# Kernel optimization log

Measured on AMD Instinct MI355X. Metric: run time of the kernel, lower is better.

## Reference

```python
import jax, jax.numpy as jnp
import numpy as np

N, D, C = 16384, 2048, 2048


def setup_inputs() -> dict:
    key = jax.random.key(0)
    k1, k2, k3, k4 = jax.random.split(key, 4)
    inputs = jax.random.normal(k1, (N, D), dtype=jnp.float32)
    centers = jax.random.normal(k2, (C, D), dtype=jnp.float32)
    # fit() sets gamma = 1/(n_features * var); emulate a small positive scalar
    gamma = jax.random.uniform(k3, (1,), dtype=jnp.float32) / D
    normalization = jax.random.normal(k4, (C, C), dtype=jnp.float32) / jnp.sqrt(jnp.float32(C))
    return {"inputs": inputs, "centers": centers, "gamma": gamma, "normalization": normalization}


def reference(inputs, centers, gamma, normalization):
    x = inputs.reshape(inputs.shape[0], -1)
    x_sq = jnp.sum(x * x, axis=1, keepdims=True)          # [N, 1]
    c_sq = jnp.sum(centers * centers, axis=1)[None, :]    # [1, C]
    sq_dists = x_sq + c_sq - 2.0 * (x @ centers.T)        # [N, C]
    densities = jnp.exp(-gamma[0] * sq_dists)             # Gaussian kernel
    return densities @ normalization                      # [N, C]
```

## Files before the change

### kernel.cpp

```cpp
#include <hip/hip_runtime.h>
#include <hip/hip_bf16.h>


#define N_ROWS 16384
#define D_DIM  2048
#define C_DIM  2048

typedef __attribute__((ext_vector_type(4))) float f32x4;
typedef __attribute__((ext_vector_type(8))) _Float16 f16x8;

__device__ __forceinline__ void load_lds16(const void* g, void* l) {
  __builtin_amdgcn_global_load_lds(
      (const __attribute__((address_space(1))) unsigned int*)g,
      (__attribute__((address_space(3))) unsigned int*)l, 16, 0, 0);
}

__global__ void prep_rows(const float* __restrict__ src,
                          _Float16* __restrict__ dst,
                          float* __restrict__ sq) {
  const int row = blockIdx.x;
  const int t = threadIdx.x;
  const float* p = src + (size_t)row * D_DIM + t * 8;
  float4 v0 = ((const float4*)p)[0];
  float4 v1 = ((const float4*)p)[1];
  float vals[8] = {v0.x, v0.y, v0.z, v0.w, v1.x, v1.y, v1.z, v1.w};
  float ss = 0.f;
  f16x8 h;
#pragma unroll
  for (int j = 0; j < 8; ++j) {
    ss += vals[j] * vals[j];
    h[j] = (_Float16)vals[j];
  }
  *(f16x8*)(dst + (size_t)row * D_DIM + t * 8) = h;
  __shared__ float red[4];
  const int lane = t & 63, wave = t >> 6;
#pragma unroll
  for (int off = 32; off > 0; off >>= 1) ss += __shfl_down(ss, off);
  if (lane == 0) red[wave] = ss;
  __syncthreads();
  if (t == 0) sq[row] = red[0] + red[1] + red[2] + red[3];
}

__global__ void prep_wt(const float* __restrict__ W,
                        _Float16* __restrict__ WT) {
  __shared__ float tile[64][65];
  const int bc = blockIdx.x >> 5;
  const int bj = blockIdx.x & 31;
  const int t = threadIdx.x;
#pragma unroll
  for (int i = 0; i < 16; ++i) {
    int idx = i * 256 + t;
    int r = idx >> 6, c = idx & 63;
    tile[r][c] = W[(size_t)(bc * 64 + r) * C_DIM + bj * 64 + c];
  }
  __syncthreads();
#pragma unroll
  for (int i = 0; i < 16; ++i) {
    int idx = i * 256 + t;
    int r2 = idx >> 6, c2 = idx & 63;
    WT[(size_t)(bj * 64 + r2) * C_DIM + bc * 64 + c2] = (_Float16)tile[c2][r2];
  }
}

__global__ __launch_bounds__(256, 2) void gemm1(
    const _Float16* __restrict__ Xh, const _Float16* __restrict__ Ch,
    const float* __restrict__ x_sq, const float* __restrict__ c_sq,
    const float* __restrict__ gamma,
    _Float16* __restrict__ Ph) {
  constexpr int K = D_DIM;
  __shared__ _Float16 As[128 * 64];
  __shared__ _Float16 Bs[128 * 64];
  const int tid = threadIdx.x;
  const int lane = tid & 63, wave = tid >> 6;
  const int wr = wave >> 1, wc = wave & 1;
  const int nwg = gridDim.x;
  const int cpx = nwg >> 3;
  const int wgid = (blockIdx.x & 7) * cpx + (blockIdx.x >> 3);
  const int bcol = wgid & 15;
  const int brow = wgid >> 4;
  const int fr = lane & 15, fq = lane >> 4;
  f32x4 acc[4][4] = {};
  const float g = gamma[0];

  const char* Abase = (const char*)(Xh + (size_t)brow * 128 * K);
  const char* Bbase = (const char*)(Ch + (size_t)bcol * 128 * K);
  for (int kt = 0; kt < K; kt += 64) {
#pragma unroll
    for (int r = 0; r < 4; ++r) {
      int base = r * 4096 + wave * 1024;
      int bo = base + lane * 16;
      int row = bo >> 7;
      int inrow = (bo & 127) ^ ((row & 7) << 4);
      load_lds16(Abase + (size_t)row * K * 2 + kt * 2 + inrow, (char*)As + base);
      load_lds16(Bbase + (size_t)row * K * 2 + kt * 2 + inrow, (char*)Bs + base);
    }
    __syncthreads();
#pragma unroll
    for (int ks = 0; ks < 64; ks += 32) {
      f16x8 af[4], bfr[4];
#pragma unroll
      for (int m = 0; m < 4; ++m) {
        int row = wr * 64 + m * 16 + fr;
        int pb = row * 128 + (((ks + fq * 8) * 2) ^ ((row & 7) << 4));
        af[m] = *(const f16x8*)((const char*)As + pb);
      }
#pragma unroll
      for (int n = 0; n < 4; ++n) {
        int row = wc * 64 + n * 16 + fr;
        int pb = row * 128 + (((ks + fq * 8) * 2) ^ ((row & 7) << 4));
        bfr[n] = *(const f16x8*)((const char*)Bs + pb);
      }
#pragma unroll
      for (int m = 0; m < 4; ++m)
#pragma unroll
        for (int n = 0; n < 4; ++n)
          acc[m][n] = __builtin_amdgcn_mfma_f32_16x16x32_f16(af[m], bfr[n], acc[m][n], 0, 0, 0);
    }
    __syncthreads();
  }
#pragma unroll
  for (int m = 0; m < 4; ++m) {
#pragma unroll
    for (int i = 0; i < 4; ++i) {
      int grow = brow * 128 + wr * 64 + m * 16 + fq * 4 + i;
      float xs = x_sq[grow];
#pragma unroll
      for (int n = 0; n < 4; ++n) {
        int gcol = bcol * 128 + wc * 64 + n * 16 + fr;
        float s = acc[m][n][i];
        float dist = xs + c_sq[gcol] - 2.0f * s;
        float p = __expf(-g * dist);
        Ph[(size_t)grow * C_DIM + gcol] = (_Float16)p;
      }
    }
  }
}

__global__ __launch_bounds__(256, 2) void gemm2(
    const _Float16* __restrict__ Ph, const _Float16* __restrict__ WT,
    float* __restrict__ out) {
  constexpr int K = C_DIM;
  __shared__ _Float16 As[128 * 64];
  __shared__ _Float16 Bs[128 * 64];
  const int tid = threadIdx.x;
  const int lane = tid & 63, wave = tid >> 6;
  const int wr = wave >> 1, wc = wave & 1;
  const int nwg = gridDim.x;
  const int cpx = nwg >> 3;
  const int wgid = (blockIdx.x & 7) * cpx + (blockIdx.x >> 3);
  const int bcol = wgid & 15;
  const int brow = wgid >> 4;
  const int fr = lane & 15, fq = lane >> 4;
  f32x4 acc[4][4] = {};

  const char* Abase = (const char*)(Ph + (size_t)brow * 128 * K);
  const char* Bbase = (const char*)(WT + (size_t)bcol * 128 * K);
  for (int kt = 0; kt < K; kt += 64) {
#pragma unroll
    for (int r = 0; r < 4; ++r) {
      int base = r * 4096 + wave * 1024;
      int bo = base + lane * 16;
      int row = bo >> 7;
      int inrow = (bo & 127) ^ ((row & 7) << 4);
      load_lds16(Abase + (size_t)row * K * 2 + kt * 2 + inrow, (char*)As + base);
      load_lds16(Bbase + (size_t)row * K * 2 + kt * 2 + inrow, (char*)Bs + base);
    }
    __syncthreads();
#pragma unroll
    for (int ks = 0; ks < 64; ks += 32) {
      f16x8 af[4], bfr[4];
#pragma unroll
      for (int m = 0; m < 4; ++m) {
        int row = wr * 64 + m * 16 + fr;
        int pb = row * 128 + (((ks + fq * 8) * 2) ^ ((row & 7) << 4));
        af[m] = *(const f16x8*)((const char*)As + pb);
      }
#pragma unroll
      for (int n = 0; n < 4; ++n) {
        int row = wc * 64 + n * 16 + fr;
        int pb = row * 128 + (((ks + fq * 8) * 2) ^ ((row & 7) << 4));
        bfr[n] = *(const f16x8*)((const char*)Bs + pb);
      }
#pragma unroll
      for (int m = 0; m < 4; ++m)
#pragma unroll
        for (int n = 0; n < 4; ++n)
          acc[m][n] = __builtin_amdgcn_mfma_f32_16x16x32_f16(af[m], bfr[n], acc[m][n], 0, 0, 0);
    }
    __syncthreads();
  }
#pragma unroll
  for (int m = 0; m < 4; ++m) {
#pragma unroll
    for (int i = 0; i < 4; ++i) {
      int grow = brow * 128 + wr * 64 + m * 16 + fq * 4 + i;
#pragma unroll
      for (int n = 0; n < 4; ++n) {
        int gcol = bcol * 128 + wc * 64 + n * 16 + fr;
        out[(size_t)grow * C_DIM + gcol] = acc[m][n][i];
      }
    }
  }
}

extern "C" void kernel_launch(void* const* d_in, const int* in_sizes, int n_in,
                              void* d_out, int out_size, void* d_ws, size_t ws_size,
                              hipStream_t stream) {
  const float* X = (const float*)d_in[0];
  const float* Cen = (const float*)d_in[1];
  const float* gamma = (const float*)d_in[2];
  const float* W = (const float*)d_in[3];
  float* out = (float*)d_out;

  char* ws = (char*)d_ws;
  _Float16* Xh = (_Float16*)ws;  ws += (size_t)N_ROWS * D_DIM * 2;
  _Float16* Ch = (_Float16*)ws;  ws += (size_t)C_DIM * D_DIM * 2;
  _Float16* WT = (_Float16*)ws;  ws += (size_t)C_DIM * C_DIM * 2;
  _Float16* Ph = (_Float16*)ws;  ws += (size_t)N_ROWS * C_DIM * 2;
  float* x_sq = (float*)ws;      ws += (size_t)N_ROWS * 4;
  float* c_sq = (float*)ws;      ws += (size_t)C_DIM * 4;

  prep_rows<<<N_ROWS, 256, 0, stream>>>(X, Xh, x_sq);
  prep_rows<<<C_DIM, 256, 0, stream>>>(Cen, Ch, c_sq);
  prep_wt<<<(C_DIM / 64) * (C_DIM / 64), 256, 0, stream>>>(W, WT);
  gemm1<<<(N_ROWS / 128) * (C_DIM / 128), 256, 0, stream>>>(Xh, Ch, x_sq, c_sq, gamma, Ph);
  gemm2<<<(N_ROWS / 128) * (C_DIM / 128), 256, 0, stream>>>(Ph, WT, out);
}
```

Before: 513.8 us.

## Use 256x256 tiles with a 4-stage async LDS pipeline in both GEMMs

Both GEMMs move to 256x256 output tiles per 512-thread workgroup, with a shared core that keeps a 4-slot ring of 32-wide K tiles in 128KB of dynamic LDS. Loads are issued three stages ahead, with explicit vmcnt waits and a single barrier per step, to overlap global-to-LDS copies with MFMA work and raise arithmetic intensity. prep_rows now handles one row per wave and drops the LDS reduction. The cost is much larger LDS use and register pressure (8x4 accumulators), which limits how many workgroups fit per CU, and the grid shrinks to 512 blocks.

Measured after the change: 509.8 us. No clear change (-0.8%).

```diff
diff --git a/kernel.cpp b/kernel.cpp
--- a/kernel.cpp
+++ b/kernel.cpp
@@ -5,9 +5,12 @@
 #define N_ROWS 16384
 #define D_DIM  2048
 #define C_DIM  2048
+#define KBYTES (D_DIM * 2)
+#define NT     64
 
 typedef __attribute__((ext_vector_type(4))) float f32x4;
 typedef __attribute__((ext_vector_type(8))) _Float16 f16x8;
+typedef __attribute__((ext_vector_type(4))) _Float16 f16x4;
 
 __device__ __forceinline__ void load_lds16(const void* g, void* l) {
   __builtin_amdgcn_global_load_lds(
@@ -18,27 +21,23 @@
 __global__ void prep_rows(const float* __restrict__ src,
                           _Float16* __restrict__ dst,
                           float* __restrict__ sq) {
-  const int row = blockIdx.x;
-  const int t = threadIdx.x;
-  const float* p = src + (size_t)row * D_DIM + t * 8;
-  float4 v0 = ((const float4*)p)[0];
-  float4 v1 = ((const float4*)p)[1];
-  float vals[8] = {v0.x, v0.y, v0.z, v0.w, v1.x, v1.y, v1.z, v1.w};
+  const int wid = threadIdx.x >> 6, lane = threadIdx.x & 63;
+  const int row = blockIdx.x * 4 + wid;
+  const float4* p = (const float4*)(src + (size_t)row * D_DIM);
+  _Float16* d = dst + (size_t)row * D_DIM;
   float ss = 0.f;
-  f16x8 h;
-#pragma unroll
-  for (int j = 0; j < 8; ++j) {
-    ss += vals[j] * vals[j];
-    h[j] = (_Float16)vals[j];
-  }
-  *(f16x8*)(dst + (size_t)row * D_DIM + t * 8) = h;
-  __shared__ float red[4];
-  const int lane = t & 63, wave = t >> 6;
+#pragma unroll
+  for (int rep = 0; rep < 8; ++rep) {
+    float4 v = p[rep * 64 + lane];
+    ss += v.x * v.x + v.y * v.y + v.z * v.z + v.w * v.w;
+    f16x4 h;
+    h[0] = (_Float16)v.x; h[1] = (_Float16)v.y;
+    h[2] = (_Float16)v.z; h[3] = (_Float16)v.w;
+    *(f16x4*)(d + (rep * 64 + lane) * 4) = h;
+  }
 #pragma unroll
   for (int off = 32; off > 0; off >>= 1) ss += __shfl_down(ss, off);
-  if (lane == 0) red[wave] = ss;
-  __syncthreads();
-  if (t == 0) sq[row] = red[0] + red[1] + red[2] + red[3];
+  if (lane == 0) sq[row] = ss;
 }
 
 __global__ void prep_wt(const float* __restrict__ W,
@@ -62,141 +61,148 @@
   }
 }
 
-__global__ __launch_bounds__(256, 2) void gemm1(
+__device__ __forceinline__ void gemm_core(
+    const char* Abase, const char* Bbase, char* smem,
+    int wid, int lane, f32x4 (&acc)[8][4]) {
+  const int wm = wid >> 2, wn = wid & 3;
+  const int fr = lane & 15, fq = lane >> 4;
+  int srcoff[2], dstoff[2];
+#pragma unroll
+  for (int q = 0; q < 2; ++q) {
+    int d = q * 8192 + wid * 1024 + lane * 16;
+    int line = d >> 7;
+    int un = (d & 127) ^ ((line & 7) << 4);
+    int r = line * 2 + (un >> 6);
+    srcoff[q] = r * KBYTES + (un & 63);
+    dstoff[q] = q * 8192 + wid * 1024;
+  }
+  int aoff[8], boff[4];
+#pragma unroll
+  for (int m = 0; m < 8; ++m) {
+    int r = wm * 128 + m * 16 + fr;
+    int line = r >> 1;
+    aoff[m] = line * 128 + ((((r & 1) << 6) | (fq << 4)) ^ ((line & 7) << 4));
+  }
+#pragma unroll
+  for (int n = 0; n < 4; ++n) {
+    int r = wn * 64 + n * 16 + fr;
+    int line = r >> 1;
+    boff[n] = line * 128 + ((((r & 1) << 6) | (fq << 4)) ^ ((line & 7) << 4));
+  }
+  char* As = smem;
+  char* Bs = smem + 65536;
+  for (int tt = 0; tt < 3; ++tt) {
+#pragma unroll
+    for (int q = 0; q < 2; ++q) {
+      load_lds16(Abase + (size_t)(srcoff[q] + tt * 64), As + tt * 16384 + dstoff[q]);
+      load_lds16(Bbase + (size_t)(srcoff[q] + tt * 64), Bs + tt * 16384 + dstoff[q]);
+    }
+  }
+  for (int t = 0; t < NT; ++t) {
+    int rem = NT - 1 - t;
+    if (rem >= 2)      asm volatile("s_waitcnt vmcnt(8)" ::: "memory");
+    else if (rem == 1) asm volatile("s_waitcnt vmcnt(4)" ::: "memory");
+    else               asm volatile("s_waitcnt vmcnt(0)" ::: "memory");
+    __builtin_amdgcn_sched_barrier(0);
+    __builtin_amdgcn_s_barrier();
+    __builtin_amdgcn_sched_barrier(0);
+    if (t + 3 < NT) {
+      int ns = (t + 3) & 3;
+#pragma unroll
+      for (int q = 0; q < 2; ++q) {
+        load_lds16(Abase + (size_t)(srcoff[q] + (t + 3) * 64), As + ns * 16384 + dstoff[q]);
+        load_lds16(Bbase + (size_t)(srcoff[q] + (t + 3) * 64), Bs + ns * 16384 + dstoff[q]);
+      }
+    }
+    __builtin_amdgcn_sched_barrier(0);
+    const char* Aslot = As + (t & 3) * 16384;
+    const char* Bslot = Bs + (t & 3) * 16384;
+    f16x8 b0 = *(const f16x8*)(Bslot + boff[0]);
+    f16x8 b1 = *(const f16x8*)(Bslot + boff[1]);
+    f16x8 b2 = *(const f16x8*)(Bslot + boff[2]);
+    f16x8 b3 = *(const f16x8*)(Bslot + boff[3]);
+    __builtin_amdgcn_s_setprio(1);
+#pragma unroll
+    for (int m = 0; m < 8; ++m) {
+      f16x8 a = *(const f16x8*)(Aslot + aoff[m]);
+      acc[m][0] = __builtin_amdgcn_mfma_f32_16x16x32_f16(a, b0, acc[m][0], 0, 0, 0);
+      acc[m][1] = __builtin_amdgcn_mfma_f32_16x16x32_f16(a, b1, acc[m][1], 0, 0, 0);
+      acc[m][2] = __builtin_amdgcn_mfma_f32_16x16x32_f16(a, b2, acc[m][2], 0, 0, 0);
+      acc[m][3] = __builtin_amdgcn_mfma_f32_16x16x32_f16(a, b3, acc[m][3], 0, 0, 0);
+    }
+    __builtin_amdgcn_s_setprio(0);
+  }
+}
+
+__global__ __launch_bounds__(512, 2) void gemm1(
     const _Float16* __restrict__ Xh, const _Float16* __restrict__ Ch,
     const float* __restrict__ x_sq, const float* __restrict__ c_sq,
     const float* __restrict__ gamma,
     _Float16* __restrict__ Ph) {
-  constexpr int K = D_DIM;
-  __shared__ _Float16 As[128 * 64];
-  __shared__ _Float16 Bs[128 * 64];
+  extern __shared__ char smem[];
   const int tid = threadIdx.x;
-  const int lane = tid & 63, wave = tid >> 6;
-  const int wr = wave >> 1, wc = wave & 1;
+  const int lane = tid & 63, wid = tid >> 6;
   const int nwg = gridDim.x;
   const int cpx = nwg >> 3;
   const int wgid = (blockIdx.x & 7) * cpx + (blockIdx.x >> 3);
-  const int bcol = wgid & 15;
-  const int brow = wgid >> 4;
+  const int bcol = wgid & 7;
+  const int brow = wgid >> 3;
+  const int wm = wid >> 2, wn = wid & 3;
   const int fr = lane & 15, fq = lane >> 4;
-  f32x4 acc[4][4] = {};
+  f32x4 acc[8][4] = {};
   const float g = gamma[0];
 
-  const char* Abase = (const char*)(Xh + (size_t)brow * 128 * K);
-  const char* Bbase = (const char*)(Ch + (size_t)bcol * 128 * K);
-  for (int kt = 0; kt < K; kt += 64) {
-#pragma unroll
-    for (int r = 0; r < 4; ++r) {
-      int base = r * 4096 + wave * 1024;
-      int bo = base + lane * 16;
-      int row = bo >> 7;
-      int inrow = (bo & 127) ^ ((row & 7) << 4);
-      load_lds16(Abase + (size_t)row * K * 2 + kt * 2 + inrow, (char*)As + base);
-      load_lds16(Bbase + (size_t)row * K * 2 + kt * 2 + inrow, (char*)Bs + base);
-    }
-    __syncthreads();
-#pragma unroll
-    for (int ks = 0; ks < 64; ks += 32) {
-      f16x8 af[4], bfr[4];
-#pragma unroll
-      for (int m = 0; m < 4; ++m) {
-        int row = wr * 64 + m * 16 + fr;
-        int pb = row * 128 + (((ks + fq * 8) * 2) ^ ((row & 7) << 4));
-        af[m] = *(const f16x8*)((const char*)As + pb);
+  gemm_core((const char*)(Xh + (size_t)brow * 256 * D_DIM),
+            (const char*)(Ch + (size_t)bcol * 256 * D_DIM),
+            smem, wid, lane, acc);
+
+  float cs[4];
+#pragma unroll
+  for (int n = 0; n < 4; ++n)
+    cs[n] = c_sq[bcol * 256 + wn * 64 + n * 16 + fr];
+#pragma unroll
+  for (int m = 0; m < 8; ++m) {
+#pragma unroll
+    for (int i = 0; i < 4; ++i) {
+      int grow = brow * 256 + wm * 128 + m * 16 + fq * 4 + i;
+      float xs = x_sq[grow];
+#pragma unroll
+      for (int n = 0; n < 4; ++n) {
+        int gcol = bcol * 256 + wn * 64 + n * 16 + fr;
+        float dist = xs + cs[n] - 2.0f * acc[m][n][i];
+        Ph[(size_t)grow * C_DIM + gcol] = (_Float16)__expf(-g * dist);
       }
-#pragma unroll
-      for (int n = 0; n < 4; ++n) {
-        int row = wc * 64 + n * 16 + fr;
-        int pb = row * 128 + (((ks + fq * 8) * 2) ^ ((row & 7) << 4));
-        bfr[n] = *(const f16x8*)((const char*)Bs + pb);
-      }
-#pragma unroll
-      for (int m = 0; m < 4; ++m)
-#pragma unroll
-        for (int n = 0; n < 4; ++n)
-          acc[m][n] = __builtin_amdgcn_mfma_f32_16x16x32_f16(af[m], bfr[n], acc[m][n], 0, 0, 0);
-    }
-    __syncthreads();
-  }
-#pragma unroll
-  for (int m = 0; m < 4; ++m) {
-#pragma unroll
-    for (int i = 0; i < 4; ++i) {
-      int grow = brow * 128 + wr * 64 + m * 16 + fq * 4 + i;
-      float xs = x_sq[grow];
-#pragma unroll
-      for (int n = 0; n < 4; ++n) {
-        int gcol = bcol * 128 + wc * 64 + n * 16 + fr;
-        float s = acc[m][n][i];
-        float dist = xs + c_sq[gcol] - 2.0f * s;
-        float p = __expf(-g * dist);
-        Ph[(size_t)grow * C_DIM + gcol] = (_Float16)p;
-      }
-    }
-  }
-}
-
-__global__ __launch_bounds__(256, 2) void gemm2(
+    }
+  }
+}
+
+__global__ __launch_bounds__(512, 2) void gemm2(
     const _Float16* __restrict__ Ph, const _Float16* __restrict__ WT,
     float* __restrict__ out) {
-  constexpr int K = C_DIM;
-  __shared__ _Float16 As[128 * 64];
-  __shared__ _Float16 Bs[128 * 64];
+  extern __shared__ char smem[];
   const int tid = threadIdx.x;
-  const int lane = tid & 63, wave = tid >> 6;
-  const int wr = wave >> 1, wc = wave & 1;
+  const int lane = tid & 63, wid = tid >> 6;
   const int nwg = gridDim.x;
   const int cpx = nwg >> 3;
   const int wgid = (blockIdx.x & 7) * cpx + (blockIdx.x >> 3);
-  const int bcol = wgid & 15;
-  const int brow = wgid >> 4;
+  const int bcol = wgid & 7;
+  const int brow = wgid >> 3;
+  const int wm = wid >> 2, wn = wid & 3;
   const int fr = lane & 15, fq = lane >> 4;
-  f32x4 acc[4][4] = {};
-
-  const char* Abase = (const char*)(Ph + (size_t)brow * 128 * K);
-  const char* Bbase = (const char*)(WT + (size_t)bcol * 128 * K);
-  for (int kt = 0; kt < K; kt += 64) {
-#pragma unroll
-    for (int r = 0; r < 4; ++r) {
-      int base = r * 4096 + wave * 1024;
-      int bo = base + lane * 16;
-      int row = bo >> 7;
-      int inrow = (bo & 127) ^ ((row & 7) << 4);
-      load_lds16(Abase + (size_t)row * K * 2 + kt * 2 + inrow, (char*)As + base);
-      load_lds16(Bbase + (size_t)row * K * 2 + kt * 2 + inrow, (char*)Bs + base);
-    }
-    __syncthreads();
-#pragma unroll
-    for (int ks = 0; ks < 64; ks += 32) {
-      f16x8 af[4], bfr[4];
-#pragma unroll
-      for (int m = 0; m < 4; ++m) {
-        int row = wr * 64 + m * 16 + fr;
-        int pb = row * 128 + (((ks + fq * 8) * 2) ^ ((row & 7) << 4));
-        af[m] = *(const f16x8*)((const char*)As + pb);
-      }
+  f32x4 acc[8][4] = {};
+
+  gemm_core((const char*)(Ph + (size_t)brow * 256 * C_DIM),
+            (const char*)(WT + (size_t)bcol * 256 * C_DIM),
+            smem, wid, lane, acc);
+
+#pragma unroll
+  for (int m = 0; m < 8; ++m) {
+#pragma unroll
+    for (int i = 0; i < 4; ++i) {
+      int grow = brow * 256 + wm * 128 + m * 16 + fq * 4 + i;
 #pragma unroll
       for (int n = 0; n < 4; ++n) {
-        int row = wc * 64 + n * 16 + fr;
-        int pb = row * 128 + (((ks + fq * 8) * 2) ^ ((row & 7) << 4));
-        bfr[n] = *(const f16x8*)((const char*)Bs + pb);
-      }
-#pragma unroll
-      for (int m = 0; m < 4; ++m)
-#pragma unroll
-        for (int n = 0; n < 4; ++n)
-          acc[m][n] = __builtin_amdgcn_mfma_f32_16x16x32_f16(af[m], bfr[n], acc[m][n], 0, 0, 0);
-    }
-    __syncthreads();
-  }
-#pragma unroll
-  for (int m = 0; m < 4; ++m) {
-#pragma unroll
-    for (int i = 0; i < 4; ++i) {
-      int grow = brow * 128 + wr * 64 + m * 16 + fq * 4 + i;
-#pragma unroll
-      for (int n = 0; n < 4; ++n) {
-        int gcol = bcol * 128 + wc * 64 + n * 16 + fr;
+        int gcol = bcol * 256 + wn * 64 + n * 16 + fr;
         out[(size_t)grow * C_DIM + gcol] = acc[m][n][i];
       }
     }
@@ -220,9 +226,14 @@
   float* x_sq = (float*)ws;      ws += (size_t)N_ROWS * 4;
   float* c_sq = (float*)ws;      ws += (size_t)C_DIM * 4;
 
-  prep_rows<<<N_ROWS, 256, 0, stream>>>(X, Xh, x_sq);
-  prep_rows<<<C_DIM, 256, 0, stream>>>(Cen, Ch, c_sq);
+  (void)hipFuncSetAttribute((const void*)gemm1,
+      hipFuncAttributeMaxDynamicSharedMemorySize, 131072);
+  (void)hipFuncSetAttribute((const void*)gemm2,
+      hipFuncAttributeMaxDynamicSharedMemorySize, 131072);
+
+  prep_rows<<<N_ROWS / 4, 256, 0, stream>>>(X, Xh, x_sq);
+  prep_rows<<<C_DIM / 4, 256, 0, stream>>>(Cen, Ch, c_sq);
   prep_wt<<<(C_DIM / 64) * (C_DIM / 64), 256, 0, stream>>>(W, WT);
-  gemm1<<<(N_ROWS / 128) * (C_DIM / 128), 256, 0, stream>>>(Xh, Ch, x_sq, c_sq, gamma, Ph);
-  gemm2<<<(N_ROWS / 128) * (C_DIM / 128), 256, 0, stream>>>(Ph, WT, out);
-}
+  gemm1<<<(N_ROWS / 256) * (C_DIM / 256), 512, 131072, stream>>>(Xh, Ch, x_sq, c_sq, gamma, Ph);
+  gemm2<<<(N_ROWS / 256) * (C_DIM / 256), 512, 131072, stream>>>(Ph, WT, out);
+}
```
